# Kernel optimization log

Measured on AMD Instinct MI355X. Metric: run time of the kernel, lower is better.

## Reference

```python
import jax, jax.numpy as jnp
import numpy as np

N = 100000      # nodes
E = 1600000     # edges
NODE_DIM = 128
HID = 128
L = 3           # num_layers
B = 512         # graphs in batch
EPS = 1e-5      # LayerNorm eps


def setup_inputs() -> dict:
    key = jax.random.key(0)
    ks = jax.random.split(key, 8)
    nodes = jax.random.normal(ks[0], (N, NODE_DIM), jnp.float32)
    edges = jax.random.randint(ks[1], (2, E), 0, N, dtype=jnp.int32)
    edge_types = jax.random.randint(ks[2], (E,), 0, 10, dtype=jnp.int32)
    batch_idx = jnp.sort(jax.random.randint(ks[3], (N,), 0, B, dtype=jnp.int32))
    w_in = jax.random.normal(ks[4], (NODE_DIM, HID), jnp.float32) / np.sqrt(NODE_DIM)
    b_in = jnp.zeros((HID,), jnp.float32)
    gcn_w = jax.random.normal(ks[5], (L, HID, HID), jnp.float32) / np.sqrt(HID)
    gcn_b = jnp.zeros((L, HID), jnp.float32)
    ln_g = jnp.ones((L, HID), jnp.float32)
    ln_b = jnp.zeros((L, HID), jnp.float32)
    return {"nodes": nodes, "edges": edges, "edge_types": edge_types,
            "batch_idx": batch_idx, "w_in": w_in, "b_in": b_in,
            "gcn_w": gcn_w, "gcn_b": gcn_b, "ln_g": ln_g, "ln_b": ln_b}


def _layer_norm(x, g, b):
    mu = jnp.mean(x, axis=-1, keepdims=True)
    var = jnp.mean(jnp.square(x - mu), axis=-1, keepdims=True)
    return (x - mu) * jax.lax.rsqrt(var + EPS) * g + b


def reference(nodes, edges, edge_types, batch_idx, w_in, b_in, gcn_w, gcn_b, ln_g, ln_b):
    src, dst = edges[0], edges[1]
    # GCN normalization with self-loops: deg = in-degree(A) + 1
    deg = jax.ops.segment_sum(jnp.ones((E,), nodes.dtype), dst, num_segments=N) + 1.0
    dinv_sqrt = jax.lax.rsqrt(deg)
    dinv = 1.0 / deg                       # self-loop norm = 1/deg_i
    enorm = dinv_sqrt[src] * dinv_sqrt[dst]

    x = nodes @ w_in + b_in                # input projection [N, HID]
    for i in range(L):
        res = x
        xw = x @ gcn_w[i]
        agg = jax.ops.segment_sum(xw[src] * enorm[:, None], dst, num_segments=N)
        x = agg + xw * dinv[:, None] + gcn_b[i]
        x = jax.nn.relu(_layer_norm(x, ln_g[i], ln_b[i]))
        # dropout is identity in eval mode
        if i > 0:
            x = x + res                    # residual only for i > 0

    # global mean pool per graph
    counts = jax.ops.segment_sum(jnp.ones((N,), x.dtype), batch_idx, num_segments=B)
    plan = jax.ops.segment_sum(x, batch_idx, num_segments=B) / jnp.maximum(counts, 1.0)[:, None]
    return x, plan
```

## Files before the change

kernel.cpp:

```cpp
#include <hip/hip_runtime.h>
#include <hip/hip_bf16.h>

typedef __attribute__((ext_vector_type(8))) short bf16x8;
typedef __attribute__((ext_vector_type(4))) float f32x4;
typedef __attribute__((ext_vector_type(2))) float f32x2;

#define K1_TILE 4096
#define NBCAP 4608

__device__ __forceinline__ unsigned short f2bf(float f) {
    union { unsigned int i; float f; } x; x.f = f;
    unsigned int r = (x.i + 0x7fffu + ((x.i >> 16) & 1u)) >> 16;
    return (unsigned short)r;
}
__device__ __forceinline__ float blo(unsigned int u) { return __uint_as_float(u << 16); }
__device__ __forceinline__ float bhi(unsigned int u) { return __uint_as_float(u & 0xffff0000u); }


__global__ __launch_bounds__(512) void bin2_k(const int* __restrict__ src,
                                              const int* __restrict__ dst,
                                              int* __restrict__ bucket_cursor,
                                              int* __restrict__ bins,
                                              int E, int NB,
                                              const float* __restrict__ w_in,
                                              const float* __restrict__ gcn_w,
                                              unsigned short* __restrict__ Wp) {
    __shared__ int hist[512];
    __shared__ int gdiff[512];
    __shared__ int wsum[8];
    __shared__ int stage[K1_TILE];
    __shared__ unsigned short sbucket[K1_TILE];
    int tid = threadIdx.x;
    int base = blockIdx.x * K1_TILE;
    int cnt = min(K1_TILE, E - base);

    hist[tid] = 0;
    __syncthreads();
    for (int i = tid; i < cnt; i += 512) atomicAdd(&hist[dst[base + i] >> 8], 1);
    __syncthreads();

    int v = hist[tid];
    int lane = tid & 63, wid = tid >> 6;
    int s = v;
#pragma unroll
    for (int o = 1; o < 64; o <<= 1) { int n = __shfl_up(s, o); if (lane >= o) s += n; }
    if (lane == 63) wsum[wid] = s;
    __syncthreads();
    if (tid == 0) { int r = 0; for (int w = 0; w < 8; ++w) { int t2 = wsum[w]; wsum[w] = r; r += t2; } }
    __syncthreads();
    int lb = s + wsum[wid] - v;
    int gb = 0;
    if (v > 0 && tid < NB) gb = atomicAdd(&bucket_cursor[tid], v);
    __syncthreads();
    hist[tid] = lb;
    gdiff[tid] = gb - lb;
    __syncthreads();

    for (int i = tid; i < cnt; i += 512) {
        int sv = src[base + i], dv = dst[base + i];
        int b = dv >> 8;
        int pos = atomicAdd(&hist[b], 1);
        stage[pos] = ((dv & 255) << 24) | sv;
        sbucket[pos] = (unsigned short)b;
    }
    __syncthreads();

    for (int i = tid; i < cnt; i += 512) {
        int lo = sbucket[i];
        int p = gdiff[lo] + i;
        if (p < NBCAP) bins[(size_t)lo * NBCAP + p] = stage[i];
    }

    if (blockIdx.x < 16) {
        int t = blockIdx.x * 512 + tid;
        int mat = t >> 11;
        int kb = (t >> 9) & 3;
        int ct = (t >> 6) & 7;
        int ln = t & 63;
        int q = ln >> 4, c = ln & 15;
        const float* W = (mat == 0) ? w_in : (gcn_w + (size_t)(mat - 1) * 16384);
        unsigned short o[8];
#pragma unroll
        for (int j = 0; j < 8; ++j)
            o[j] = f2bf(W[(size_t)(kb * 32 + q * 8 + j) * 128 + ct * 16 + c]);
        unsigned short* dstp = Wp + ((size_t)t) * 8;
#pragma unroll
        for (int j = 0; j < 8; ++j) dstp[j] = o[j];
    }
}


__global__ __launch_bounds__(512) void csr_build_k(const int* __restrict__ bins,
                                                   const int* __restrict__ bucket_cursor,
                                                   int* __restrict__ csr_src,
                                                   int* __restrict__ row_start,
                                                   float* __restrict__ dinv_sqrt,
                                                   float* __restrict__ dinv,
                                                   int N, int NB) {
    __shared__ int counts[256];
    __shared__ int cursor[256];
    __shared__ int wsum[8];
    __shared__ int bbase[512];
    __shared__ int lcsr[NBCAP];
    int b = blockIdx.x, tid = threadIdx.x;
    int lane = tid & 63, wid = tid >> 6;

    {
        int v = (tid < NB) ? min(bucket_cursor[tid], NBCAP) : 0;
        int s = v;
#pragma unroll
        for (int o = 1; o < 64; o <<= 1) { int n = __shfl_up(s, o); if (lane >= o) s += n; }
        if (lane == 63) wsum[wid] = s;
        __syncthreads();
        if (tid == 0) { int r = 0; for (int w = 0; w < 8; ++w) { int t2 = wsum[w]; wsum[w] = r; r += t2; } }
        __syncthreads();
        bbase[tid] = s + wsum[wid] - v;
    }
    __syncthreads();
    int cbase = bbase[b];
    int cnt = min(bucket_cursor[b], NBCAP);
    const int* my = bins + (size_t)b * NBCAP;
    __syncthreads();

    if (tid < 256) counts[tid] = 0;
    __syncthreads();
    for (int i = tid; i < cnt; i += 512) atomicAdd(&counts[((unsigned)my[i]) >> 24], 1);
    __syncthreads();

    int v = (tid < 256) ? counts[tid] : 0;
    int s = v;
#pragma unroll
    for (int o = 1; o < 64; o <<= 1) { int n = __shfl_up(s, o); if (lane >= o) s += n; }
    if (lane == 63) wsum[wid] = s;
    __syncthreads();
    if (tid == 0) { int r = 0; for (int w = 0; w < 8; ++w) { int t2 = wsum[w]; wsum[w] = r; r += t2; } }
    __syncthreads();
    int excl = s + wsum[wid] - v;

    if (tid < 256) {
        int node = b * 256 + tid;
        if (node <= N) row_start[node] = cbase + excl;
        if (node < N) {
            float dg = (float)v + 1.0f;
            dinv_sqrt[node] = rsqrtf(dg);
            dinv[node] = 1.0f / dg;
        }
        cursor[tid] = excl;
    }
    __syncthreads();

    for (int i = tid; i < cnt; i += 512) {
        int e = my[i];
        int pos = atomicAdd(&cursor[((unsigned)e) >> 24], 1);
        lcsr[pos] = e & 0xffffff;
    }
    __syncthreads();
    for (int i = tid; i < cnt; i += 512) csr_src[cbase + i] = lcsr[i];
}


__global__ __launch_bounds__(256) void proj_k(const float* __restrict__ A,
                                              const unsigned short* __restrict__ Wp,
                                              const float* __restrict__ bias,
                                              unsigned short* __restrict__ Cb,
                                              int M) {
    __shared__ unsigned short stage[64 * 128];
    int wid = threadIdx.x >> 6, lane = threadIdx.x & 63;
    int blk0 = blockIdx.x * 64;
    int r0 = blk0 + wid * 16;
    int q = lane >> 4, c = lane & 15;
    int ar = min(r0 + c, M - 1);

    f32x4 acc[8];
#pragma unroll
    for (int ct = 0; ct < 8; ++ct) acc[ct] = (f32x4){0.f, 0.f, 0.f, 0.f};

#pragma unroll
    for (int kb = 0; kb < 4; ++kb) {
        float4 f0 = *(const float4*)&A[(size_t)ar * 128 + kb * 32 + q * 8];
        float4 f1 = *(const float4*)&A[(size_t)ar * 128 + kb * 32 + q * 8 + 4];
        union { unsigned short u[8]; bf16x8 v; } af;
        af.u[0] = f2bf(f0.x); af.u[1] = f2bf(f0.y); af.u[2] = f2bf(f0.z); af.u[3] = f2bf(f0.w);
        af.u[4] = f2bf(f1.x); af.u[5] = f2bf(f1.y); af.u[6] = f2bf(f1.z); af.u[7] = f2bf(f1.w);
#pragma unroll
        for (int ct = 0; ct < 8; ++ct) {
            bf16x8 b = *(const bf16x8*)&Wp[(((size_t)(kb * 8 + ct)) * 64 + lane) * 8];
            acc[ct] = __builtin_amdgcn_mfma_f32_16x16x32_bf16(af.v, b, acc[ct], 0, 0, 0);
        }
    }

#pragma unroll
    for (int ct = 0; ct < 8; ++ct) {
        int col = ct * 16 + c;
        float bv = bias[col];
#pragma unroll
        for (int r = 0; r < 4; ++r)
            stage[(wid * 16 + q * 4 + r) * 128 + col] = f2bf(acc[ct][r] + bv);
    }
    __syncthreads();

    int tid = threadIdx.x;
#pragma unroll
    for (int i = 0; i < 4; ++i) {
        int k = tid + i * 256;
        int row = k >> 4, colc = (k & 15) * 8;
        int grow = blk0 + row;
        if (grow < M)
            *(uint4*)&Cb[(size_t)grow * 128 + colc] = *(const uint4*)&stage[row * 128 + colc];
    }
}


__global__ __launch_bounds__(256) void gemmln_k(const unsigned short* __restrict__ S,
                                                unsigned short* xb16,
                                                float* __restrict__ xout,
                                                const unsigned short* __restrict__ Wp,
                                                const float* __restrict__ bias,
                                                const float* __restrict__ g,
                                                const float* __restrict__ bb,
                                                int M, int residual, int write_f32) {
    __shared__ unsigned short stage[64 * 128];
    int wid = threadIdx.x >> 6, lane = threadIdx.x & 63;
    int blk0 = blockIdx.x * 64;
    int r0 = blk0 + wid * 16;
    int q = lane >> 4, c = lane & 15;
    int ar = min(r0 + c, M - 1);

    f32x4 acc[8];
#pragma unroll
    for (int ct = 0; ct < 8; ++ct) acc[ct] = (f32x4){0.f, 0.f, 0.f, 0.f};

#pragma unroll
    for (int kb = 0; kb < 4; ++kb) {
        bf16x8 a = *(const bf16x8*)&S[(size_t)ar * 128 + kb * 32 + q * 8];
#pragma unroll
        for (int ct = 0; ct < 8; ++ct) {
            bf16x8 b = *(const bf16x8*)&Wp[(((size_t)(kb * 8 + ct)) * 64 + lane) * 8];
            acc[ct] = __builtin_amdgcn_mfma_f32_16x16x32_bf16(a, b, acc[ct], 0, 0, 0);
        }
    }

    float v[8][4];
#pragma unroll
    for (int ct = 0; ct < 8; ++ct) {
        float bv = bias[ct * 16 + c];
#pragma unroll
        for (int r = 0; r < 4; ++r) v[ct][r] = acc[ct][r] + bv;
    }

    float mu[4], rs[4];
#pragma unroll
    for (int r = 0; r < 4; ++r) {
        float s = 0.f;
#pragma unroll
        for (int ct = 0; ct < 8; ++ct) s += v[ct][r];
        s += __shfl_xor(s, 1); s += __shfl_xor(s, 2);
        s += __shfl_xor(s, 4); s += __shfl_xor(s, 8);
        mu[r] = s * (1.0f / 128.0f);
    }
#pragma unroll
    for (int r = 0; r < 4; ++r) {
        float s = 0.f;
#pragma unroll
        for (int ct = 0; ct < 8; ++ct) { float d = v[ct][r] - mu[r]; s += d * d; }
        s += __shfl_xor(s, 1); s += __shfl_xor(s, 2);
        s += __shfl_xor(s, 4); s += __shfl_xor(s, 8);
        rs[r] = rsqrtf(s * (1.0f / 128.0f) + 1e-5f);
    }

#pragma unroll
    for (int ct = 0; ct < 8; ++ct) {
        int col = ct * 16 + c;
        float gamma = g[col], beta = bb[col];
#pragma unroll
        for (int r = 0; r < 4; ++r) {
            float y = fmaxf((v[ct][r] - mu[r]) * rs[r] * gamma + beta, 0.f);
            stage[(wid * 16 + q * 4 + r) * 128 + col] = f2bf(y);
        }
    }
    __syncthreads();

    int tid = threadIdx.x;
#pragma unroll
    for (int i = 0; i < 4; ++i) {
        int k = tid + i * 256;
        int row = k >> 4, colc = (k & 15) * 8;
        int grow = blk0 + row;
        if (grow >= M) continue;
        uint4 sv = *(const uint4*)&stage[row * 128 + colc];
        float y0 = blo(sv.x), y1 = bhi(sv.x), y2 = blo(sv.y), y3 = bhi(sv.y);
        float y4 = blo(sv.z), y5 = bhi(sv.z), y6 = blo(sv.w), y7 = bhi(sv.w);
        if (residual) {
            uint4 rv = *(const uint4*)&xb16[(size_t)grow * 128 + colc];
            y0 += blo(rv.x); y1 += bhi(rv.x); y2 += blo(rv.y); y3 += bhi(rv.y);
            y4 += blo(rv.z); y5 += bhi(rv.z); y6 += blo(rv.w); y7 += bhi(rv.w);
        }
        union { unsigned short u[8]; uint4 qv; } o;
        o.u[0] = f2bf(y0); o.u[1] = f2bf(y1); o.u[2] = f2bf(y2); o.u[3] = f2bf(y3);
        o.u[4] = f2bf(y4); o.u[5] = f2bf(y5); o.u[6] = f2bf(y6); o.u[7] = f2bf(y7);
        *(uint4*)&xb16[(size_t)grow * 128 + colc] = o.qv;
        if (write_f32) {
            *(float4*)&xout[(size_t)grow * 128 + colc] = make_float4(y0, y1, y2, y3);
            *(float4*)&xout[(size_t)grow * 128 + colc + 4] = make_float4(y4, y5, y6, y7);
        }
    }
}


__device__ __forceinline__ void acc8(f32x2& a0, f32x2& a1, f32x2& a2, f32x2& a3,
                                     uint4 u, float w) {
    f32x2 w2 = {w, w};
    f32x2 p0 = {blo(u.x), bhi(u.x)};
    f32x2 p1 = {blo(u.y), bhi(u.y)};
    f32x2 p2 = {blo(u.z), bhi(u.z)};
    f32x2 p3 = {blo(u.w), bhi(u.w)};
    a0 += p0 * w2; a1 += p1 * w2; a2 += p2 * w2; a3 += p3 * w2;
}

__global__ __launch_bounds__(256) void agg_k(const unsigned short* __restrict__ xb16,
                                             unsigned short* __restrict__ S,
                                             const int* __restrict__ row_start,
                                             const int* __restrict__ csr_src,
                                             const float* __restrict__ dst_tbl,
                                             const float* __restrict__ dinv,
                                             int N) {
    int wid = threadIdx.x >> 6, lane = threadIdx.x & 63;
    int n = blockIdx.x * 4 + wid;
    if (n >= N) return;
    int grp = lane >> 4;
    int sl = lane & 15;
    int c0 = sl * 8;

    int beg = row_start[n], end = row_start[n + 1];
    int deg = end - beg;

    int pidx = 0; float pw = 0.f;
    if (lane < deg) {
        pidx = csr_src[beg + lane];
        pw = dst_tbl[pidx];
    }

    f32x2 a0 = {0.f, 0.f}, a1 = {0.f, 0.f}, a2 = {0.f, 0.f}, a3 = {0.f, 0.f};

    int dcap = min(deg, 64);
    for (int j = 0; j < dcap; j += 16) {
        int e0 = j + grp, e1 = e0 + 4, e2 = e0 + 8, e3 = e0 + 12;
        int s0 = __shfl(pidx, e0); float w0 = __shfl(pw, e0);
        int s1 = __shfl(pidx, e1); float w1 = __shfl(pw, e1);
        int s2 = __shfl(pidx, e2); float w2 = __shfl(pw, e2);
        int s3 = __shfl(pidx, e3); float w3 = __shfl(pw, e3);
        uint4 u0 = *(const uint4*)(xb16 + (s0 * 128 + c0));
        uint4 u1 = *(const uint4*)(xb16 + (s1 * 128 + c0));
        uint4 u2 = *(const uint4*)(xb16 + (s2 * 128 + c0));
        uint4 u3 = *(const uint4*)(xb16 + (s3 * 128 + c0));
        acc8(a0, a1, a2, a3, u0, w0);
        acc8(a0, a1, a2, a3, u1, w1);
        acc8(a0, a1, a2, a3, u2, w2);
        acc8(a0, a1, a2, a3, u3, w3);
    }

    for (int j = 64; j < deg; j += 8) {
        int ja = j + grp, jb = j + grp + 4;
        int sa = csr_src[beg + min(ja, deg - 1)];
        int sb = csr_src[beg + min(jb, deg - 1)];
        float wa = (ja < deg) ? dst_tbl[sa] : 0.f;
        float wb = (jb < deg) ? dst_tbl[sb] : 0.f;
        uint4 ua = *(const uint4*)(xb16 + (sa * 128 + c0));
        uint4 ub = *(const uint4*)(xb16 + (sb * 128 + c0));
        acc8(a0, a1, a2, a3, ua, wa);
        acc8(a0, a1, a2, a3, ub, wb);
    }

#pragma unroll
    for (int o = 16; o <= 32; o <<= 1) {
        a0.x += __shfl_xor(a0.x, o); a0.y += __shfl_xor(a0.y, o);
        a1.x += __shfl_xor(a1.x, o); a1.y += __shfl_xor(a1.y, o);
        a2.x += __shfl_xor(a2.x, o); a2.y += __shfl_xor(a2.y, o);
        a3.x += __shfl_xor(a3.x, o); a3.y += __shfl_xor(a3.y, o);
    }

    if (grp == 0) {
        float dsd = dst_tbl[n];
        float di = dinv[n];
        uint4 u = *(const uint4*)(xb16 + (n * 128 + c0));
        float y0 = a0.x * dsd + blo(u.x) * di;
        float y1 = a0.y * dsd + bhi(u.x) * di;
        float y2 = a1.x * dsd + blo(u.y) * di;
        float y3 = a1.y * dsd + bhi(u.y) * di;
        float y4 = a2.x * dsd + blo(u.z) * di;
        float y5 = a2.y * dsd + bhi(u.z) * di;
        float y6 = a3.x * dsd + blo(u.w) * di;
        float y7 = a3.y * dsd + bhi(u.w) * di;
        union { unsigned short us[8]; uint4 qv; } o;
        o.us[0] = f2bf(y0); o.us[1] = f2bf(y1); o.us[2] = f2bf(y2); o.us[3] = f2bf(y3);
        o.us[4] = f2bf(y4); o.us[5] = f2bf(y5); o.us[6] = f2bf(y6); o.us[7] = f2bf(y7);
        *(uint4*)(S + (n * 128 + c0)) = o.qv;
    }
}


__global__ __launch_bounds__(256) void pool_k(const unsigned short* __restrict__ x,
                                              const int* __restrict__ bidx,
                                              float* __restrict__ plan, int N) {
    __shared__ float red[8 * 128];
    __shared__ int se[2];
    int b = blockIdx.x, t = threadIdx.x;

    if (t < 2) {
        int target = b + t;
        int lo = 0, hi = N;
        while (lo < hi) { int mid = (lo + hi) >> 1; if (bidx[mid] < target) lo = mid + 1; else hi = mid; }
        se[t] = lo;
    }
    __syncthreads();
    int s = se[0], e = se[1];

    int cg = (t & 31) * 4;
    int h = t >> 5;
    float acc0 = 0.f, acc1 = 0.f, acc2 = 0.f, acc3 = 0.f;
    for (int i = s + h; i < e; i += 8) {
        uint2 u = *(const uint2*)&x[(size_t)i * 128 + cg];
        acc0 += blo(u.x); acc1 += bhi(u.x); acc2 += blo(u.y); acc3 += bhi(u.y);
    }
    red[h * 128 + cg] = acc0; red[h * 128 + cg + 1] = acc1;
    red[h * 128 + cg + 2] = acc2; red[h * 128 + cg + 3] = acc3;
    __syncthreads();
    if (h == 0) {
#pragma unroll
        for (int k = 1; k < 8; ++k) {
            acc0 += red[k * 128 + cg];     acc1 += red[k * 128 + cg + 1];
            acc2 += red[k * 128 + cg + 2]; acc3 += red[k * 128 + cg + 3];
        }
        float inv = 1.0f / (float)max(e - s, 1);
        *(float4*)&plan[(size_t)b * 128 + cg] = make_float4(acc0 * inv, acc1 * inv,
                                                            acc2 * inv, acc3 * inv);
    }
}


extern "C" void kernel_launch(void* const* d_in, const int* in_sizes, int n_in,
                              void* d_out, int out_size, void* d_ws, size_t ws_size,
                              hipStream_t stream) {
    const float* nodes     = (const float*)d_in[0];
    const int*   edges     = (const int*)d_in[1];
    const int*   batch_idx = (const int*)d_in[3];
    const float* w_in      = (const float*)d_in[4];
    const float* b_in      = (const float*)d_in[5];
    const float* gcn_w     = (const float*)d_in[6];
    const float* gcn_b     = (const float*)d_in[7];
    const float* ln_g      = (const float*)d_in[8];
    const float* ln_b      = (const float*)d_in[9];

    const int N = in_sizes[0] / 128;
    const int E = in_sizes[1] / 2;
    const int B = out_size / 128 - N;
    const int* src = edges;
    const int* dst = edges + E;
    const int NB = (N + 256) / 256;

    float* xbuf = (float*)d_out;
    float* plan = xbuf + (size_t)N * 128;

    unsigned short* xb16 = (unsigned short*)d_ws;
    unsigned short* Sb   = xb16 + (size_t)N * 128;
    unsigned short* Wp   = Sb + (size_t)N * 128;
    int* bins            = (int*)(Wp + 4 * 16384);
    int* bucket_cursor   = bins + (size_t)NB * NBCAP;
    int* csr_src         = bucket_cursor + 512;
    int* row_start       = csr_src + E;
    float* dinv_sqrt     = (float*)(row_start + N + 1);
    float* dinv          = dinv_sqrt + N;

    hipMemsetAsync(bucket_cursor, 0, sizeof(int) * NB, stream);

    bin2_k<<<(E + K1_TILE - 1) / K1_TILE, 512, 0, stream>>>(src, dst, bucket_cursor, bins,
                                                            E, NB, w_in, gcn_w, Wp);
    csr_build_k<<<NB, 512, 0, stream>>>(bins, bucket_cursor,
                                        csr_src, row_start, dinv_sqrt, dinv, N, NB);

    proj_k<<<(N + 63) / 64, 256, 0, stream>>>(nodes, Wp, b_in, xb16, N);

    for (int l = 0; l < 3; ++l) {
        agg_k<<<(N + 3) / 4, 256, 0, stream>>>(xb16, Sb, row_start, csr_src,
                                               dinv_sqrt, dinv, N);
        gemmln_k<<<(N + 63) / 64, 256, 0, stream>>>(Sb, xb16, xbuf,
                                                    Wp + (size_t)(l + 1) * 16384,
                                                    gcn_b + (size_t)l * 128,
                                                    ln_g + (size_t)l * 128,
                                                    ln_b + (size_t)l * 128, N,
                                                    l > 0 ? 1 : 0, l == 2 ? 1 : 0);
    }

    pool_k<<<B, 256, 0, stream>>>(xb16, batch_idx, plan, N);
}
```

Measured before the change: 418.9 us.

## Fuse mean-pool accumulation into final GEMM-LN and scatter bins directly

The final gemmln layer now accumulates per-graph sums into shared-memory partial buckets keyed by graph id and flushes them to the pooled output with global atomics. A light normalization kernel then divides by the node counts. This removes the separate pool pass that re-read the bf16 activations, and the final layer no longer writes the bf16 copy. Separately, the binning kernel writes each edge directly to its global bin position instead of staging in shared memory first, which drops one barrier and the LDS buffers but loses write coalescing. The pooled sums now use float atomics, so their rounding order is no longer deterministic.

```diff
diff --git a/kernel.cpp b/kernel.cpp
--- a/kernel.cpp
+++ b/kernel.cpp
@@ -7,6 +7,7 @@
 
 #define K1_TILE 4096
 #define NBCAP 4608
+#define GMAX 16
 
 __device__ __forceinline__ unsigned short f2bf(float f) {
     union { unsigned int i; float f; } x; x.f = f;
@@ -26,10 +27,8 @@
                                               const float* __restrict__ gcn_w,
                                               unsigned short* __restrict__ Wp) {
     __shared__ int hist[512];
-    __shared__ int gdiff[512];
+    __shared__ int gbase[512];
     __shared__ int wsum[8];
-    __shared__ int stage[K1_TILE];
-    __shared__ unsigned short sbucket[K1_TILE];
     int tid = threadIdx.x;
     int base = blockIdx.x * K1_TILE;
     int cnt = min(K1_TILE, E - base);
@@ -53,22 +52,15 @@
     if (v > 0 && tid < NB) gb = atomicAdd(&bucket_cursor[tid], v);
     __syncthreads();
     hist[tid] = lb;
-    gdiff[tid] = gb - lb;
+    gbase[tid] = gb - lb;
     __syncthreads();
 
     for (int i = tid; i < cnt; i += 512) {
         int sv = src[base + i], dv = dst[base + i];
         int b = dv >> 8;
         int pos = atomicAdd(&hist[b], 1);
-        stage[pos] = ((dv & 255) << 24) | sv;
-        sbucket[pos] = (unsigned short)b;
-    }
-    __syncthreads();
-
-    for (int i = tid; i < cnt; i += 512) {
-        int lo = sbucket[i];
-        int p = gdiff[lo] + i;
-        if (p < NBCAP) bins[(size_t)lo * NBCAP + p] = stage[i];
+        int gp = gbase[b] + pos;
+        if (gp < NBCAP) bins[(size_t)b * NBCAP + gp] = ((dv & 255) << 24) | sv;
     }
 
     if (blockIdx.x < 16) {
@@ -218,13 +210,24 @@
                                                 const float* __restrict__ bias,
                                                 const float* __restrict__ g,
                                                 const float* __restrict__ bb,
-                                                int M, int residual, int write_f32) {
+                                                const int* __restrict__ bidx,
+                                                float* __restrict__ plan,
+                                                int M, int residual, int final_layer) {
     __shared__ unsigned short stage[64 * 128];
+    __shared__ float pacc[GMAX * 128];
+    __shared__ int gid0s;
     int wid = threadIdx.x >> 6, lane = threadIdx.x & 63;
     int blk0 = blockIdx.x * 64;
     int r0 = blk0 + wid * 16;
     int q = lane >> 4, c = lane & 15;
     int ar = min(r0 + c, M - 1);
+    int tid = threadIdx.x;
+
+    if (final_layer) {
+#pragma unroll
+        for (int i = 0; i < GMAX * 128 / 256; ++i) pacc[tid + i * 256] = 0.f;
+        if (tid == 0) gid0s = bidx[min(blk0, M - 1)];
+    }
 
     f32x4 acc[8];
 #pragma unroll
@@ -280,7 +283,6 @@
     }
     __syncthreads();
 
-    int tid = threadIdx.x;
 #pragma unroll
     for (int i = 0; i < 4; ++i) {
         int k = tid + i * 256;
@@ -295,15 +297,56 @@
             y0 += blo(rv.x); y1 += bhi(rv.x); y2 += blo(rv.y); y3 += bhi(rv.y);
             y4 += blo(rv.z); y5 += bhi(rv.z); y6 += blo(rv.w); y7 += bhi(rv.w);
         }
-        union { unsigned short u[8]; uint4 qv; } o;
-        o.u[0] = f2bf(y0); o.u[1] = f2bf(y1); o.u[2] = f2bf(y2); o.u[3] = f2bf(y3);
-        o.u[4] = f2bf(y4); o.u[5] = f2bf(y5); o.u[6] = f2bf(y6); o.u[7] = f2bf(y7);
-        *(uint4*)&xb16[(size_t)grow * 128 + colc] = o.qv;
-        if (write_f32) {
+        if (!final_layer) {
+            union { unsigned short u[8]; uint4 qv; } o;
+            o.u[0] = f2bf(y0); o.u[1] = f2bf(y1); o.u[2] = f2bf(y2); o.u[3] = f2bf(y3);
+            o.u[4] = f2bf(y4); o.u[5] = f2bf(y5); o.u[6] = f2bf(y6); o.u[7] = f2bf(y7);
+            *(uint4*)&xb16[(size_t)grow * 128 + colc] = o.qv;
+        } else {
             *(float4*)&xout[(size_t)grow * 128 + colc] = make_float4(y0, y1, y2, y3);
             *(float4*)&xout[(size_t)grow * 128 + colc + 4] = make_float4(y4, y5, y6, y7);
-        }
-    }
+            int gg = bidx[grow] - gid0s;
+            if (gg < GMAX) {
+                float* p = &pacc[gg * 128 + colc];
+                atomicAdd(p + 0, y0); atomicAdd(p + 1, y1);
+                atomicAdd(p + 2, y2); atomicAdd(p + 3, y3);
+                atomicAdd(p + 4, y4); atomicAdd(p + 5, y5);
+                atomicAdd(p + 6, y6); atomicAdd(p + 7, y7);
+            } else {
+                float* p = &plan[(size_t)bidx[grow] * 128 + colc];
+                atomicAdd(p + 0, y0); atomicAdd(p + 1, y1);
+                atomicAdd(p + 2, y2); atomicAdd(p + 3, y3);
+                atomicAdd(p + 4, y4); atomicAdd(p + 5, y5);
+                atomicAdd(p + 6, y6); atomicAdd(p + 7, y7);
+            }
+        }
+    }
+
+    if (final_layer) {
+        __syncthreads();
+#pragma unroll
+        for (int i = 0; i < GMAX * 128 / 256; ++i) {
+            int k = tid + i * 256;
+            float val = pacc[k];
+            if (val != 0.f) atomicAdd(&plan[(size_t)(gid0s + (k >> 7)) * 128 + (k & 127)], val);
+        }
+    }
+}
+
+
+__global__ __launch_bounds__(128) void poolnorm_k(float* __restrict__ plan,
+                                                  const int* __restrict__ bidx, int N) {
+    __shared__ int se[2];
+    int b = blockIdx.x, t = threadIdx.x;
+    if (t < 2) {
+        int target = b + t;
+        int lo = 0, hi = N;
+        while (lo < hi) { int mid = (lo + hi) >> 1; if (bidx[mid] < target) lo = mid + 1; else hi = mid; }
+        se[t] = lo;
+    }
+    __syncthreads();
+    float inv = 1.0f / (float)max(se[1] - se[0], 1);
+    plan[(size_t)b * 128 + t] *= inv;
 }
 
 
@@ -399,45 +442,6 @@
 }
 
 
-__global__ __launch_bounds__(256) void pool_k(const unsigned short* __restrict__ x,
-                                              const int* __restrict__ bidx,
-                                              float* __restrict__ plan, int N) {
-    __shared__ float red[8 * 128];
-    __shared__ int se[2];
-    int b = blockIdx.x, t = threadIdx.x;
-
-    if (t < 2) {
-        int target = b + t;
-        int lo = 0, hi = N;
-        while (lo < hi) { int mid = (lo + hi) >> 1; if (bidx[mid] < target) lo = mid + 1; else hi = mid; }
-        se[t] = lo;
-    }
-    __syncthreads();
-    int s = se[0], e = se[1];
-
-    int cg = (t & 31) * 4;
-    int h = t >> 5;
-    float acc0 = 0.f, acc1 = 0.f, acc2 = 0.f, acc3 = 0.f;
-    for (int i = s + h; i < e; i += 8) {
-        uint2 u = *(const uint2*)&x[(size_t)i * 128 + cg];
-        acc0 += blo(u.x); acc1 += bhi(u.x); acc2 += blo(u.y); acc3 += bhi(u.y);
-    }
-    red[h * 128 + cg] = acc0; red[h * 128 + cg + 1] = acc1;
-    red[h * 128 + cg + 2] = acc2; red[h * 128 + cg + 3] = acc3;
-    __syncthreads();
-    if (h == 0) {
-#pragma unroll
-        for (int k = 1; k < 8; ++k) {
-            acc0 += red[k * 128 + cg];     acc1 += red[k * 128 + cg + 1];
-            acc2 += red[k * 128 + cg + 2]; acc3 += red[k * 128 + cg + 3];
-        }
-        float inv = 1.0f / (float)max(e - s, 1);
-        *(float4*)&plan[(size_t)b * 128 + cg] = make_float4(acc0 * inv, acc1 * inv,
-                                                            acc2 * inv, acc3 * inv);
-    }
-}
-
-
 extern "C" void kernel_launch(void* const* d_in, const int* in_sizes, int n_in,
                               void* d_out, int out_size, void* d_ws, size_t ws_size,
                               hipStream_t stream) {
@@ -472,6 +476,7 @@
     float* dinv          = dinv_sqrt + N;
 
     hipMemsetAsync(bucket_cursor, 0, sizeof(int) * NB, stream);
+    hipMemsetAsync(plan, 0, sizeof(float) * (size_t)B * 128, stream);
 
     bin2_k<<<(E + K1_TILE - 1) / K1_TILE, 512, 0, stream>>>(src, dst, bucket_cursor, bins,
                                                             E, NB, w_in, gcn_w, Wp);
@@ -487,9 +492,10 @@
                                                     Wp + (size_t)(l + 1) * 16384,
                                                     gcn_b + (size_t)l * 128,
                                                     ln_g + (size_t)l * 128,
-                                                    ln_b + (size_t)l * 128, N,
+                                                    ln_b + (size_t)l * 128,
+                                                    batch_idx, plan, N,
                                                     l > 0 ? 1 : 0, l == 2 ? 1 : 0);
     }
 
-    pool_k<<<B, 256, 0, stream>>>(xb16, batch_idx, plan, N);
-}
+    poolnorm_k<<<B, 128, 0, stream>>>(plan, batch_idx, N);
+}
```

Measured after the change: 487.4 us. 16.4% more time.
